# Optimization experiments

Hardware: AMD Instinct MI355X
Metric: run time of the kernel (lower is better)

## Reference

```python
import math
import jax, jax.numpy as jnp
import numpy as np

B, S, D, H = 2, 4096, 1024, 16
HD = D // H            # 64 head dim
FFN = 4096             # encoder_ffn_dim = 4*d_model
WIN = 512              # attention_window
w = WIN // 2           # one-sided window = 256
NEG = -1e9


def setup_inputs() -> dict:
    key = jax.random.key(0)
    ks = jax.random.split(key, 16)
    p = lambda k, shape: (jax.random.normal(k, shape, jnp.float32) * 0.02)
    inp = {
        "hidden_states": jax.random.normal(ks[0], (B, S, D), jnp.float32),
        "attention_mask": jnp.zeros((B, S), jnp.float32),
        "layer_head_mask": jnp.ones((H,), jnp.float32),
        "is_index_masked": jnp.zeros((B, S), bool),
        "is_index_global_attn": jnp.zeros((B, S), bool),
        "is_global_attn": 0,
        "Wq": p(ks[1], (D, D)), "bq": jnp.zeros((D,), jnp.float32),
        "Wk": p(ks[2], (D, D)), "bk": jnp.zeros((D,), jnp.float32),
        "Wv": p(ks[3], (D, D)), "bv": jnp.zeros((D,), jnp.float32),
        "Wo": p(ks[4], (D, D)), "bo": jnp.zeros((D,), jnp.float32),
        "ln1_g": jnp.ones((D,), jnp.float32), "ln1_b": jnp.zeros((D,), jnp.float32),
        "W1": p(ks[5], (D, FFN)), "b1": jnp.zeros((FFN,), jnp.float32),
        "W2": p(ks[6], (FFN, D)), "b2": jnp.zeros((D,), jnp.float32),
        "ln2_g": jnp.ones((D,), jnp.float32), "ln2_b": jnp.zeros((D,), jnp.float32),
    }
    return inp


def _ln(x, g, b, eps=1e-5):
    m = x.mean(-1, keepdims=True)
    v = ((x - m) ** 2).mean(-1, keepdims=True)
    return (x - m) * jax.lax.rsqrt(v + eps) * g + b


def _blocks3(x, nb, pad_val=0.0):
    # x: [B, H, S, d] -> [B, H, nb, 3w, d]: key blocks b-1, b, b+1 per query block b
    xp = jnp.pad(x, ((0, 0), (0, 0), (w, w), (0, 0)), constant_values=pad_val)
    xb = xp.reshape(x.shape[0], x.shape[1], nb + 2, w, x.shape[-1])
    return jnp.concatenate([xb[:, :, i:i + nb] for i in range(3)], axis=3)


def _sliding_window_attn(q, k, v, key_mask_add, is_masked_q, head_mask):
    # q,k,v: [B, H, S, hd]; banded attention |i-j| <= w
    b, h, s, hd = q.shape
    nb = s // w
    qb = (q * (1.0 / math.sqrt(hd))).reshape(b, h, nb, w, hd)
    kb = _blocks3(k, nb)
    vb = _blocks3(v, nb)
    scores = jnp.einsum("bhnqd,bhnkd->bhnqk", qb, kb)  # [B,H,nb,w,3w]
    # additive key mask (padding keys get NEG)
    kmp = jnp.pad(key_mask_add, ((0, 0), (w, w)), constant_values=NEG)
    kmp = kmp.reshape(b, nb + 2, w)
    km = jnp.concatenate([kmp[:, i:i + nb] for i in range(3)], axis=2)  # [B,nb,3w]
    scores = scores + km[:, None, :, None, :]
    qi = jnp.arange(w)[:, None]
    ki = jnp.arange(3 * w)[None, :]
    band = jnp.abs(ki - w - qi) <= w  # [w, 3w]
    scores = jnp.where(band, scores, NEG)
    probs = jax.nn.softmax(scores, axis=-1)
    probs = probs * head_mask[None, :, None, None, None]
    probs = jnp.where(is_masked_q.reshape(b, 1, nb, w, 1), 0.0, probs)
    out = jnp.einsum("bhnqk,bhnkd->bhnqd", probs, vb)
    return out.reshape(b, h, s, hd)


def reference(hidden_states, attention_mask, layer_head_mask, is_index_masked,
              is_index_global_attn, is_global_attn,
              Wq, bq, Wk, bk, Wv, bv, Wo, bo, ln1_g, ln1_b,
              W1, b1, W2, b2, ln2_g, ln2_b):
    hs = hidden_states
    split = lambda x: (x).reshape(B, S, H, HD).transpose(0, 2, 1, 3)  # [B,H,S,hd]
    q = split(hs @ Wq + bq)
    k = split(hs @ Wk + bk)
    v = split(hs @ Wv + bv)
    attn = _sliding_window_attn(q, k, v, attention_mask, is_index_masked, layer_head_mask)
    attn = attn.transpose(0, 2, 1, 3).reshape(B, S, D)
    attn = attn @ Wo + bo  # self_attn output projection
    x = _ln(hs + attn, ln1_g, ln1_b)
    h = jax.nn.gelu(x @ W1 + b1, approximate=False)
    h = h @ W2 + b2
    x = _ln(x + h, ln2_g, ln2_b)
    return x
```

## Files before the change

kernel.cpp:

```cpp
#include <hip/hip_runtime.h>


typedef unsigned short ushort_t;
typedef unsigned char uchar_t;
typedef __attribute__((ext_vector_type(8))) short bf16x8;
typedef __attribute__((ext_vector_type(4))) float f32x4;

constexpr int CB  = 2;
constexpr int CS  = 4096;
constexpr int CD  = 1024;
constexpr int CH  = 16;
constexpr int CHD = 64;
constexpr int CF  = 4096;
constexpr int CM  = CB * CS;
constexpr float NEGV = -1e9f;

__device__ __forceinline__ ushort_t f2bf(float f) {
  unsigned u = __float_as_uint(f);
  unsigned r = u + 0x7FFFu + ((u >> 16) & 1u);
  return (ushort_t)(r >> 16);
}
__device__ __forceinline__ float gelu_exact(float x) {
  return 0.5f * x * (1.0f + erff(x * 0.70710678118654752f));
}

__device__ __forceinline__ bf16x8 ldsfrag(const char* lds, int row, int slot) {
  return *(const bf16x8*)(lds + row * 128 + (((slot ^ (row & 7)) << 4)));
}

template <int NROWS>
__device__ __forceinline__ void stage_swz(const ushort_t* __restrict__ src, int stride,
                                          char* lds, int tid) {
  const int lane = tid & 63, w = tid >> 6;
#pragma unroll
  for (int it = 0; it < NROWS / 32; ++it) {
    const int o   = it * 4096 + w * 1024;
    const int eo  = o + lane * 16;
    const int row = eo >> 7;
    const int lslot = ((eo >> 4) & 7) ^ (row & 7);
    const ushort_t* g = src + (size_t)row * stride + lslot * 8;
    __builtin_amdgcn_global_load_lds((const __attribute__((address_space(1))) void*)g,
                                     (__attribute__((address_space(3))) void*)(lds + o),
                                     16, 0, 0);
  }
}

__device__ __forceinline__ void stageC(const ushort_t* __restrict__ gtile, int ldK,
                                       char* ldsT, int chunk, int tid) {
  const int eo   = chunk * 8192 + tid * 16;
  const int row  = eo >> 7;
  const int slot = ((eo >> 4) & 7) ^ (row & 7);
  __builtin_amdgcn_global_load_lds(
      (const __attribute__((address_space(1))) void*)(gtile + (size_t)row * ldK + slot * 8),
      (__attribute__((address_space(3))) void*)(ldsT + eo), 16, 0, 0);
}

template <int MH, int NH, int NPH, int NF, int VM, typename F>
__device__ __forceinline__ void phase8(const char* Ax, const char* Bx,
                                       int wr, int wc, int rl, int kl,
                                       f32x4 (&acc)[8][NF], F stage) {
  bf16x8 af[4][2], bfr[NPH][2];
#pragma unroll
  for (int mf = 0; mf < 4; ++mf)
#pragma unroll
    for (int kk = 0; kk < 2; ++kk)
      af[mf][kk] = ldsfrag(Ax, wr * 128 + (MH * 4 + mf) * 16 + rl, kk * 4 + kl);
#pragma unroll
  for (int nf = 0; nf < NPH; ++nf)
#pragma unroll
    for (int kk = 0; kk < 2; ++kk)
      bfr[nf][kk] = ldsfrag(Bx, wc * (NF * 16) + (NH * NPH + nf) * 16 + rl, kk * 4 + kl);
  stage();
  __builtin_amdgcn_s_barrier();
  asm volatile("s_waitcnt lgkmcnt(0)" ::: "memory");
  __builtin_amdgcn_s_setprio(1);
#pragma unroll
  for (int mf = 0; mf < 4; ++mf)
#pragma unroll
    for (int nf = 0; nf < NPH; ++nf)
#pragma unroll
      for (int kk = 0; kk < 2; ++kk)
        acc[MH * 4 + mf][NH * NPH + nf] = __builtin_amdgcn_mfma_f32_16x16x32_bf16(
            af[mf][kk], bfr[nf][kk], acc[MH * 4 + mf][NH * NPH + nf], 0, 0, 0);
  __builtin_amdgcn_s_setprio(0);
  if constexpr (VM == 1) asm volatile("s_waitcnt vmcnt(2)" ::: "memory");
  if constexpr (VM == 2) asm volatile("s_waitcnt vmcnt(0)" ::: "memory");
  __builtin_amdgcn_s_barrier();
}

template <int BN>
__device__ __forceinline__ void run_mainloop(const ushort_t* __restrict__ A,
                                             const ushort_t* __restrict__ Bt,
                                             int K, int bm, int bn, char* lds, int tid,
                                             f32x4 (&acc)[8][BN / 64]) {
  constexpr int NF = BN / 64;
  char* Ab0 = lds;
  char* Bb0 = lds + 32768;
  char* Ab1 = lds + 32768 + BN * 128;
  char* Bb1 = Ab1 + 32768;
  const int lane = tid & 63, wid = tid >> 6;
  const int wr = wid >> 2, wc = wid & 3, rl = lane & 15, kl = lane >> 4;
  const ushort_t* Ao = A + (size_t)bm * K;
  const ushort_t* Bo = Bt + (size_t)bn * K;
  const int NT = K >> 6;
#pragma unroll
  for (int c = 0; c < 4; ++c) stageC(Ao, K, Ab0, c, tid);
#pragma unroll
  for (int c = 0; c < NF; ++c) stageC(Bo, K, Bb0, c, tid);
  if (NT > 1) {
    stageC(Ao + 64, K, Ab1, 0, tid);
    stageC(Ao + 64, K, Ab1, 2, tid);
    asm volatile("s_waitcnt vmcnt(2)" ::: "memory");
  } else {
    asm volatile("s_waitcnt vmcnt(0)" ::: "memory");
  }
  __builtin_amdgcn_s_barrier();

  for (int m = 0; m < NT; ++m) {
    const int p = m & 1;
    char* Ax = p ? Ab1 : Ab0;  char* Bx = p ? Bb1 : Bb0;
    char* Axn = p ? Ab0 : Ab1; char* Bxn = p ? Bb0 : Bb1;
    const bool s1 = (m + 1 < NT), s2 = (m + 2 < NT);
    const ushort_t* An1 = Ao + (m + 1) * 64;
    const ushort_t* Bn1 = Bo + (m + 1) * 64;
    const ushort_t* An2 = Ao + (m + 2) * 64;
    if constexpr (NF == 4) {
      phase8<0, 0, 2, 4, 0>(Ax, Bx, wr, wc, rl, kl, acc, [&] {
        if (s1) { stageC(An1, K, Axn, 1, tid); stageC(An1, K, Axn, 3, tid); } });
      phase8<0, 1, 2, 4, 0>(Ax, Bx, wr, wc, rl, kl, acc, [&] {
        if (s1) { stageC(Bn1, K, Bxn, 0, tid); stageC(Bn1, K, Bxn, 1, tid); } });
      phase8<1, 0, 2, 4, 0>(Ax, Bx, wr, wc, rl, kl, acc, [&] {
        if (s1) { stageC(Bn1, K, Bxn, 2, tid); stageC(Bn1, K, Bxn, 3, tid); } });
      if (s2)      phase8<1, 1, 2, 4, 1>(Ax, Bx, wr, wc, rl, kl, acc, [&] {
        stageC(An2, K, Ax, 0, tid); stageC(An2, K, Ax, 2, tid); });
      else if (s1) phase8<1, 1, 2, 4, 2>(Ax, Bx, wr, wc, rl, kl, acc, [&] {});
      else         phase8<1, 1, 2, 4, 0>(Ax, Bx, wr, wc, rl, kl, acc, [&] {});
    } else {
      phase8<0, 0, 2, 2, 0>(Ax, Bx, wr, wc, rl, kl, acc, [&] {
        if (s1) { stageC(An1, K, Axn, 1, tid); stageC(An1, K, Axn, 3, tid);
                  stageC(Bn1, K, Bxn, 0, tid); } });
      if (s2)      phase8<1, 0, 2, 2, 1>(Ax, Bx, wr, wc, rl, kl, acc, [&] {
        stageC(Bn1, K, Bxn, 1, tid);
        stageC(An2, K, Ax, 0, tid); stageC(An2, K, Ax, 2, tid); });
      else if (s1) phase8<1, 0, 2, 2, 2>(Ax, Bx, wr, wc, rl, kl, acc, [&] {
        stageC(Bn1, K, Bxn, 1, tid); });
      else         phase8<1, 0, 2, 2, 0>(Ax, Bx, wr, wc, rl, kl, acc, [&] {});
    }
  }
}

template <int BN, int EPI>
__global__ __launch_bounds__(512, 1) void gemm8(
    const ushort_t* __restrict__ A, const ushort_t* __restrict__ Bt,
    const float* __restrict__ bias, const float* __restrict__ res,
    float* __restrict__ outF, ushort_t* __restrict__ outB, int N, int K) {
  constexpr int NF = BN / 64;
  __shared__ __align__(16) char lds[2 * (32768 + BN * 128)];
  const int tid = threadIdx.x;
  const int bm = blockIdx.x * 256, bn = blockIdx.y * BN;
  f32x4 acc[8][NF] = {};
  run_mainloop<BN>(A, Bt, K, bm, bn, lds, tid, acc);
  const int lane = tid & 63, wid = tid >> 6;
  const int wr = wid >> 2, wc = wid & 3, rl = lane & 15, kl = lane >> 4;
#pragma unroll
  for (int mf = 0; mf < 8; ++mf) {
    const int r0 = bm + wr * 128 + mf * 16 + kl * 4;
#pragma unroll
    for (int nf = 0; nf < NF; ++nf) {
      const int col = bn + wc * (NF * 16) + nf * 16 + rl;
      const float bb = bias[col];
#pragma unroll
      for (int i = 0; i < 4; ++i) {
        float v = acc[mf][nf][i] + bb;
        if (EPI == 1) {
          v += res[(size_t)(r0 + i) * N + col];
          outF[(size_t)(r0 + i) * N + col] = v;
        } else {
          outB[(size_t)(r0 + i) * N + col] = f2bf(gelu_exact(v));
        }
      }
    }
  }
}

__global__ __launch_bounds__(512, 1) void qkv8(
    const ushort_t* __restrict__ hsb,
    const ushort_t* __restrict__ WqT, const ushort_t* __restrict__ WkT,
    const ushort_t* __restrict__ WvT,
    const float* __restrict__ bq, const float* __restrict__ bk, const float* __restrict__ bv,
    ushort_t* __restrict__ q, ushort_t* __restrict__ k, ushort_t* __restrict__ vt) {
  __shared__ __align__(16) char lds[2 * (32768 + 16384)];
  const int tid = threadIdx.x;
  const int which = blockIdx.z;
  const ushort_t* Wt = (which == 0) ? WqT : (which == 1) ? WkT : WvT;
  const float* bia   = (which == 0) ? bq  : (which == 1) ? bk  : bv;
  const float mul    = (which == 0) ? 0.125f : 1.0f;
  const int bm = blockIdx.x * 256, bn = blockIdx.y * 128;
  f32x4 acc[8][2] = {};
  run_mainloop<128>(hsb, Wt, CD, bm, bn, lds, tid, acc);
  const int lane = tid & 63, wid = tid >> 6;
  const int wr = wid >> 2, wc = wid & 3, rl = lane & 15, kl = lane >> 4;
#pragma unroll
  for (int mf = 0; mf < 8; ++mf) {
    const int r0 = bm + wr * 128 + mf * 16 + kl * 4;
    const int bidx = r0 >> 12;
    const int s0 = r0 & (CS - 1);
#pragma unroll
    for (int nf = 0; nf < 2; ++nf) {
      const int col = bn + wc * 32 + nf * 16 + rl;
      const int h = col >> 6, hd = col & 63;
      const float bb = bia[col];
      if (which < 2) {
        ushort_t* dst = (which == 0 ? q : k);
#pragma unroll
        for (int i = 0; i < 4; ++i) {
          const float v = (acc[mf][nf][i] + bb) * mul;
          dst[((((size_t)bidx * CH + h) * CS) + s0 + i) * CHD + hd] = f2bf(v);
        }
      } else {
        ushort4 o;
        o.x = f2bf(acc[mf][nf][0] + bb); o.y = f2bf(acc[mf][nf][1] + bb);
        o.z = f2bf(acc[mf][nf][2] + bb); o.w = f2bf(acc[mf][nf][3] + bb);
        *(ushort4*)&vt[(((size_t)bidx * CH + h) * CHD + hd) * CS + s0] = o;
      }
    }
  }
}

__global__ __launch_bounds__(256) void cast_bf16(const float* __restrict__ x,
                                                 ushort_t* __restrict__ y) {
  const size_t i = ((size_t)blockIdx.x * 256 + threadIdx.x) * 4;
  const float4 v = *(const float4*)(x + i);
  ushort4 o;
  o.x = f2bf(v.x); o.y = f2bf(v.y); o.z = f2bf(v.z); o.w = f2bf(v.w);
  *(ushort4*)(y + i) = o;
}

__global__ __launch_bounds__(256) void transpose_cast(const float* __restrict__ W,
                                                      ushort_t* __restrict__ Wt,
                                                      int K, int N) {
  __shared__ float t[64][65];
  const int k0 = blockIdx.x * 64, n0 = blockIdx.y * 64;
  const int ty = threadIdx.x >> 4, tx = threadIdx.x & 15;
#pragma unroll
  for (int rr = 0; rr < 4; ++rr) {
    const int r = rr * 16 + ty;
    const float4 v = *(const float4*)&W[(size_t)(k0 + r) * N + n0 + tx * 4];
    t[r][tx * 4 + 0] = v.x; t[r][tx * 4 + 1] = v.y;
    t[r][tx * 4 + 2] = v.z; t[r][tx * 4 + 3] = v.w;
  }
  __syncthreads();
#pragma unroll
  for (int rr = 0; rr < 4; ++rr) {
    const int rn = rr * 16 + ty;
    ushort4 o;
    o.x = f2bf(t[tx * 4 + 0][rn]); o.y = f2bf(t[tx * 4 + 1][rn]);
    o.z = f2bf(t[tx * 4 + 2][rn]); o.w = f2bf(t[tx * 4 + 3][rn]);
    *(ushort4*)&Wt[(size_t)(n0 + rn) * K + k0 + tx * 4] = o;
  }
}

__global__ __launch_bounds__(256) void attn_mfma(
    const ushort_t* __restrict__ qg, const ushort_t* __restrict__ kg,
    const ushort_t* __restrict__ vtg,
    const float* __restrict__ amask, const uchar_t* __restrict__ qmask,
    const float* __restrict__ hmask, ushort_t* __restrict__ outb) {
  __shared__ __align__(16) char Qs[8192];
  __shared__ __align__(16) char Ks[8192];
  __shared__ __align__(16) char Vt[8192];
  __shared__ __align__(16) char Ps[8192];
  const int qt0 = blockIdx.x * 64, h = blockIdx.y, b = blockIdx.z;
  const int tid = threadIdx.x, lane = tid & 63, w = tid >> 6;
  const size_t bh = (size_t)b * CH + h;

  stage_swz<64>(qg + (bh * CS + qt0) * CHD, CHD, Qs, tid);

  f32x4 O[4] = {};
  float m_run[4], l_run[4];
#pragma unroll
  for (int i = 0; i < 4; ++i) { m_run[i] = -INFINITY; l_run[i] = 0.f; }

  for (int c = 0; c < 9; ++c) {
    const int k0 = qt0 - 256 + c * 64;
    if (k0 < 0 || k0 >= CS) continue;
    __syncthreads();
    stage_swz<64>(kg + (bh * CS + k0) * CHD, CHD, Ks, tid);
    stage_swz<64>(vtg + bh * CHD * CS + k0, CS, Vt, tid);
    __syncthreads();

    f32x4 s[4] = {};
#pragma unroll
    for (int kk = 0; kk < 2; ++kk) {
      const bf16x8 a = ldsfrag(Qs, w * 16 + (lane & 15), kk * 4 + (lane >> 4));
#pragma unroll
      for (int n = 0; n < 4; ++n) {
        const bf16x8 bb = ldsfrag(Ks, n * 16 + (lane & 15), kk * 4 + (lane >> 4));
        s[n] = __builtin_amdgcn_mfma_f32_16x16x32_bf16(a, bb, s[n], 0, 0, 0);
      }
    }

    float kmv[4]; int keyc[4];
#pragma unroll
    for (int n = 0; n < 4; ++n) {
      keyc[n] = k0 + n * 16 + (lane & 15);
      kmv[n] = amask[(size_t)b * CS + keyc[n]];
    }
    const int qrb = qt0 + w * 16 + ((lane >> 4) << 2);
#pragma unroll
    for (int i = 0; i < 4; ++i) {
      const int qi = qrb + i;
      float mx = -INFINITY;
#pragma unroll
      for (int n = 0; n < 4; ++n) {
        const int d = keyc[n] - qi;
        float x = (d <= 256 && d >= -256) ? (s[n][i] + kmv[n]) : NEGV;
        s[n][i] = x;
        mx = fmaxf(mx, x);
      }
      mx = fmaxf(mx, __shfl_xor(mx, 1));
      mx = fmaxf(mx, __shfl_xor(mx, 2));
      mx = fmaxf(mx, __shfl_xor(mx, 4));
      mx = fmaxf(mx, __shfl_xor(mx, 8));
      const float m_new = fmaxf(m_run[i], mx);
      const float scf = expf(m_run[i] - m_new);
      float rs = 0.f;
#pragma unroll
      for (int n = 0; n < 4; ++n) {
        const float p = expf(s[n][i] - m_new);
        s[n][i] = p;
        rs += p;
      }
      rs += __shfl_xor(rs, 1); rs += __shfl_xor(rs, 2);
      rs += __shfl_xor(rs, 4); rs += __shfl_xor(rs, 8);
      l_run[i] = l_run[i] * scf + rs;
      m_run[i] = m_new;
#pragma unroll
      for (int n = 0; n < 4; ++n) O[n][i] *= scf;
      const int prow = w * 16 + ((lane >> 4) << 2) + i;
#pragma unroll
      for (int n = 0; n < 4; ++n) {
        const int pcol = n * 16 + (lane & 15);
        const int byte = prow * 128 + ((((pcol >> 3) ^ (prow & 7)) << 4)) + ((pcol & 7) << 1);
        *(ushort_t*)(Ps + byte) = f2bf(s[n][i]);
      }
    }
    __syncthreads();

#pragma unroll
    for (int kk = 0; kk < 2; ++kk) {
      const bf16x8 pa = ldsfrag(Ps, w * 16 + (lane & 15), kk * 4 + (lane >> 4));
#pragma unroll
      for (int nd = 0; nd < 4; ++nd) {
        const bf16x8 vv = ldsfrag(Vt, nd * 16 + (lane & 15), kk * 4 + (lane >> 4));
        O[nd] = __builtin_amdgcn_mfma_f32_16x16x32_bf16(pa, vv, O[nd], 0, 0, 0);
      }
    }
  }

  const float hm = hmask[h];
#pragma unroll
  for (int i = 0; i < 4; ++i) {
    const int qi = qt0 + w * 16 + ((lane >> 4) << 2) + i;
    const bool qm = qmask[(size_t)b * CS + qi] != 0;
    const float scl = (qm ? 0.f : hm) / fmaxf(l_run[i], 1e-30f);
#pragma unroll
    for (int nd = 0; nd < 4; ++nd) {
      const int col = h * CHD + nd * 16 + (lane & 15);
      outb[((size_t)b * CS + qi) * CD + col] = f2bf(O[nd][i] * scl);
    }
  }
}

__global__ __launch_bounds__(256) void ln_f32(const float* __restrict__ X,
                                              const float* __restrict__ g,
                                              const float* __restrict__ bt,
                                              float* __restrict__ Y,
                                              ushort_t* __restrict__ Yb) {
  const int row = blockIdx.x;
  const int tid = threadIdx.x;
  const float4 xv = *(const float4*)(X + (size_t)row * CD + (tid << 2));
  float s  = xv.x + xv.y + xv.z + xv.w;
  float s2 = xv.x * xv.x + xv.y * xv.y + xv.z * xv.z + xv.w * xv.w;
#pragma unroll
  for (int off = 32; off; off >>= 1) {
    s  += __shfl_xor(s, off);
    s2 += __shfl_xor(s2, off);
  }
  __shared__ float red[8];
  const int wv = tid >> 6;
  if ((tid & 63) == 0) { red[wv] = s; red[wv + 4] = s2; }
  __syncthreads();
  s  = red[0] + red[1] + red[2] + red[3];
  s2 = red[4] + red[5] + red[6] + red[7];
  const float mean = s * (1.f / CD);
  const float var  = s2 * (1.f / CD) - mean * mean;
  const float r = rsqrtf(var + 1e-5f);
  const float4 gv = *(const float4*)(g + (tid << 2));
  const float4 bv = *(const float4*)(bt + (tid << 2));
  float4 o;
  o.x = (xv.x - mean) * r * gv.x + bv.x;
  o.y = (xv.y - mean) * r * gv.y + bv.y;
  o.z = (xv.z - mean) * r * gv.z + bv.z;
  o.w = (xv.w - mean) * r * gv.w + bv.w;
  *(float4*)(Y + (size_t)row * CD + (tid << 2)) = o;
  if (Yb) {
    ushort4 ob;
    ob.x = f2bf(o.x); ob.y = f2bf(o.y); ob.z = f2bf(o.z); ob.w = f2bf(o.w);
    *(ushort4*)(Yb + (size_t)row * CD + (tid << 2)) = ob;
  }
}

extern "C" void kernel_launch(void* const* d_in, const int* in_sizes, int n_in,
                              void* d_out, int out_size, void* d_ws, size_t ws_size,
                              hipStream_t stream) {
  const float* hs    = (const float*)d_in[0];
  const float* amask = (const float*)d_in[1];
  const float* hmask = (const float*)d_in[2];
  const uchar_t* qmask = (const uchar_t*)d_in[3];
  const float* Wq = (const float*)d_in[6];
  const float* bq = (const float*)d_in[7];
  const float* Wk = (const float*)d_in[8];
  const float* bk = (const float*)d_in[9];
  const float* Wv = (const float*)d_in[10];
  const float* bv = (const float*)d_in[11];
  const float* Wo = (const float*)d_in[12];
  const float* bo = (const float*)d_in[13];
  const float* ln1g = (const float*)d_in[14];
  const float* ln1b = (const float*)d_in[15];
  const float* W1 = (const float*)d_in[16];
  const float* b1 = (const float*)d_in[17];
  const float* W2 = (const float*)d_in[18];
  const float* b2 = (const float*)d_in[19];
  const float* ln2g = (const float*)d_in[20];
  const float* ln2b = (const float*)d_in[21];

  char* ws = (char*)d_ws;
  const size_t MB = 1024 * 1024;
  ushort_t* hsb  = (ushort_t*)(ws);
  ushort_t* WqT  = (ushort_t*)(ws + 16 * MB);
  ushort_t* WkT  = (ushort_t*)(ws + 18 * MB);
  ushort_t* WvT  = (ushort_t*)(ws + 20 * MB);
  ushort_t* WoT  = (ushort_t*)(ws + 22 * MB);
  ushort_t* W1T  = (ushort_t*)(ws + 24 * MB);
  ushort_t* W2T  = (ushort_t*)(ws + 32 * MB);
  ushort_t* qb   = (ushort_t*)(ws + 40 * MB);
  ushort_t* kb   = (ushort_t*)(ws + 56 * MB);
  ushort_t* vtb  = (ushort_t*)(ws + 72 * MB);
  ushort_t* attb = (ushort_t*)(ws + 88 * MB);
  float*    tmp  = (float*)(ws + 104 * MB);
  float*    x1   = (float*)(ws + 40 * MB);
  ushort_t* x1b  = (ushort_t*)(ws + 72 * MB);
  ushort_t* hb   = (ushort_t*)(ws + 136 * MB);
  float*    outf = (float*)d_out;

  cast_bf16<<<(CM * CD) / 1024, 256, 0, stream>>>(hs, hsb);
  transpose_cast<<<dim3(CD / 64, CD / 64), 256, 0, stream>>>(Wq, WqT, CD, CD);
  transpose_cast<<<dim3(CD / 64, CD / 64), 256, 0, stream>>>(Wk, WkT, CD, CD);
  transpose_cast<<<dim3(CD / 64, CD / 64), 256, 0, stream>>>(Wv, WvT, CD, CD);
  transpose_cast<<<dim3(CD / 64, CD / 64), 256, 0, stream>>>(Wo, WoT, CD, CD);
  transpose_cast<<<dim3(CD / 64, CF / 64), 256, 0, stream>>>(W1, W1T, CD, CF);
  transpose_cast<<<dim3(CF / 64, CD / 64), 256, 0, stream>>>(W2, W2T, CF, CD);

  qkv8<<<dim3(CM / 256, CD / 128, 3), 512, 0, stream>>>(
      hsb, WqT, WkT, WvT, bq, bk, bv, qb, kb, vtb);

  attn_mfma<<<dim3(CS / 64, CH, CB), 256, 0, stream>>>(
      qb, kb, vtb, amask, qmask, hmask, attb);

  gemm8<128, 1><<<dim3(CM / 256, CD / 128), 512, 0, stream>>>(
      attb, WoT, bo, hs, tmp, nullptr, CD, CD);

  ln_f32<<<CM, 256, 0, stream>>>(tmp, ln1g, ln1b, x1, x1b);

  gemm8<256, 2><<<dim3(CM / 256, CF / 256), 512, 0, stream>>>(
      x1b, W1T, b1, nullptr, nullptr, hb, CF, CD);

  gemm8<128, 1><<<dim3(CM / 256, CD / 128), 512, 0, stream>>>(
      hb, W2T, b2, x1, outf, nullptr, CD, CF);

  ln_f32<<<CM, 256, 0, stream>>>(outf, ln2g, ln2b, outf, nullptr);
}
```

Measured before the change: 569.2 us.

## Reschedule GEMM prefetch order, add workgroup swizzle, merge QKV weights into one GEMM

Reorders the global-to-LDS staging in the GEMM mainloop so B tiles are loaded before A, and retunes the vmcnt wait thresholds per phase. For BN=256 the prefetch depth drops to a single stage with a full wait in the prologue. Adds a workgroup-ID swizzle that interleaves tiles across groups of 8, aiming at better L2 reuse across XCDs. The three QKV weights are packed into one contiguous transposed matrix so qkv8 runs as a single 2D grid. The changed waits trade deeper prefetch for simpler ordering, which risks stalls if the new vmcnt counts are off.

```diff
diff --git a/kernel.cpp b/kernel.cpp
--- a/kernel.cpp
+++ b/kernel.cpp
@@ -83,8 +83,10 @@
         acc[MH * 4 + mf][NH * NPH + nf] = __builtin_amdgcn_mfma_f32_16x16x32_bf16(
             af[mf][kk], bfr[nf][kk], acc[MH * 4 + mf][NH * NPH + nf], 0, 0, 0);
   __builtin_amdgcn_s_setprio(0);
-  if constexpr (VM == 1) asm volatile("s_waitcnt vmcnt(2)" ::: "memory");
-  if constexpr (VM == 2) asm volatile("s_waitcnt vmcnt(0)" ::: "memory");
+  if constexpr (VM == 0) asm volatile("s_waitcnt vmcnt(0)" ::: "memory");
+  if constexpr (VM == 2) asm volatile("s_waitcnt vmcnt(2)" ::: "memory");
+  if constexpr (VM == 4) asm volatile("s_waitcnt vmcnt(4)" ::: "memory");
+  if constexpr (VM == 6) asm volatile("s_waitcnt vmcnt(6)" ::: "memory");
   __builtin_amdgcn_s_barrier();
 }
 
@@ -103,16 +105,24 @@
   const ushort_t* Ao = A + (size_t)bm * K;
   const ushort_t* Bo = Bt + (size_t)bn * K;
   const int NT = K >> 6;
-#pragma unroll
-  for (int c = 0; c < 4; ++c) stageC(Ao, K, Ab0, c, tid);
-#pragma unroll
-  for (int c = 0; c < NF; ++c) stageC(Bo, K, Bb0, c, tid);
-  if (NT > 1) {
-    stageC(Ao + 64, K, Ab1, 0, tid);
-    stageC(Ao + 64, K, Ab1, 2, tid);
-    asm volatile("s_waitcnt vmcnt(2)" ::: "memory");
+
+  if constexpr (NF == 4) {
+#pragma unroll
+    for (int c = 0; c < 4; ++c) stageC(Bo, K, Bb0, c, tid);
+#pragma unroll
+    for (int c = 0; c < 4; ++c) stageC(Ao, K, Ab0, c, tid);
+    asm volatile("s_waitcnt vmcnt(0)" ::: "memory");
   } else {
-    asm volatile("s_waitcnt vmcnt(0)" ::: "memory");
+    stageC(Bo, K, Bb0, 0, tid); stageC(Bo, K, Bb0, 1, tid);
+#pragma unroll
+    for (int c = 0; c < 4; ++c) stageC(Ao, K, Ab0, c, tid);
+    if (NT > 1) {
+      stageC(Ao + 64, K, Ab1, 0, tid);
+      stageC(Ao + 64, K, Ab1, 2, tid);
+      asm volatile("s_waitcnt vmcnt(2)" ::: "memory");
+    } else {
+      asm volatile("s_waitcnt vmcnt(0)" ::: "memory");
+    }
   }
   __builtin_amdgcn_s_barrier();
 
@@ -125,28 +135,36 @@
     const ushort_t* Bn1 = Bo + (m + 1) * 64;
     const ushort_t* An2 = Ao + (m + 2) * 64;
     if constexpr (NF == 4) {
-      phase8<0, 0, 2, 4, 0>(Ax, Bx, wr, wc, rl, kl, acc, [&] {
+      phase8<0, 0, 2, 4, -1>(Ax, Bx, wr, wc, rl, kl, acc, [&] {
+        if (s1) { stageC(Bn1, K, Bxn, 0, tid); stageC(Bn1, K, Bxn, 1, tid);
+                  stageC(Bn1, K, Bxn, 2, tid); stageC(Bn1, K, Bxn, 3, tid); } });
+      if (s1) phase8<0, 1, 2, 4, 6>(Ax, Bx, wr, wc, rl, kl, acc, [&] {
+        stageC(An1, K, Axn, 0, tid); stageC(An1, K, Axn, 2, tid); });
+      else    phase8<0, 1, 2, 4, 0>(Ax, Bx, wr, wc, rl, kl, acc, [&] {});
+      phase8<1, 0, 2, 4, -1>(Ax, Bx, wr, wc, rl, kl, acc, [&] {
         if (s1) { stageC(An1, K, Axn, 1, tid); stageC(An1, K, Axn, 3, tid); } });
-      phase8<0, 1, 2, 4, 0>(Ax, Bx, wr, wc, rl, kl, acc, [&] {
-        if (s1) { stageC(Bn1, K, Bxn, 0, tid); stageC(Bn1, K, Bxn, 1, tid); } });
-      phase8<1, 0, 2, 4, 0>(Ax, Bx, wr, wc, rl, kl, acc, [&] {
-        if (s1) { stageC(Bn1, K, Bxn, 2, tid); stageC(Bn1, K, Bxn, 3, tid); } });
-      if (s2)      phase8<1, 1, 2, 4, 1>(Ax, Bx, wr, wc, rl, kl, acc, [&] {
+      if (s1) phase8<1, 1, 2, 4, 2>(Ax, Bx, wr, wc, rl, kl, acc, [&] {});
+      else    phase8<1, 1, 2, 4, 0>(Ax, Bx, wr, wc, rl, kl, acc, [&] {});
+    } else {
+      if (s1) phase8<0, 0, 2, 2, 6>(Ax, Bx, wr, wc, rl, kl, acc, [&] {
+        stageC(Bn1, K, Bxn, 0, tid); stageC(Bn1, K, Bxn, 1, tid);
+        stageC(An1, K, Axn, 1, tid); stageC(An1, K, Axn, 3, tid); });
+      else    phase8<0, 0, 2, 2, 0>(Ax, Bx, wr, wc, rl, kl, acc, [&] {});
+      if (s2)      phase8<1, 0, 2, 2, 4>(Ax, Bx, wr, wc, rl, kl, acc, [&] {
         stageC(An2, K, Ax, 0, tid); stageC(An2, K, Ax, 2, tid); });
-      else if (s1) phase8<1, 1, 2, 4, 2>(Ax, Bx, wr, wc, rl, kl, acc, [&] {});
-      else         phase8<1, 1, 2, 4, 0>(Ax, Bx, wr, wc, rl, kl, acc, [&] {});
-    } else {
-      phase8<0, 0, 2, 2, 0>(Ax, Bx, wr, wc, rl, kl, acc, [&] {
-        if (s1) { stageC(An1, K, Axn, 1, tid); stageC(An1, K, Axn, 3, tid);
-                  stageC(Bn1, K, Bxn, 0, tid); } });
-      if (s2)      phase8<1, 0, 2, 2, 1>(Ax, Bx, wr, wc, rl, kl, acc, [&] {
-        stageC(Bn1, K, Bxn, 1, tid);
-        stageC(An2, K, Ax, 0, tid); stageC(An2, K, Ax, 2, tid); });
-      else if (s1) phase8<1, 0, 2, 2, 2>(Ax, Bx, wr, wc, rl, kl, acc, [&] {
-        stageC(Bn1, K, Bxn, 1, tid); });
+      else if (s1) phase8<1, 0, 2, 2, 2>(Ax, Bx, wr, wc, rl, kl, acc, [&] {});
       else         phase8<1, 0, 2, 2, 0>(Ax, Bx, wr, wc, rl, kl, acc, [&] {});
     }
   }
+}
+
+__device__ __forceinline__ void swz_block(int BN, int& bm, int& bn) {
+  const int gx = gridDim.x;
+  const int nwg = gx * gridDim.y;
+  const int id0 = blockIdx.x + gx * blockIdx.y;
+  const int wgid = (id0 & 7) * (nwg >> 3) + (id0 >> 3);
+  bm = (wgid % gx) * 256;
+  bn = (wgid / gx) * BN;
 }
 
 template <int BN, int EPI>
@@ -157,7 +175,7 @@
   constexpr int NF = BN / 64;
   __shared__ __align__(16) char lds[2 * (32768 + BN * 128)];
   const int tid = threadIdx.x;
-  const int bm = blockIdx.x * 256, bn = blockIdx.y * BN;
+  int bm, bn; swz_block(BN, bm, bn);
   f32x4 acc[8][NF] = {};
   run_mainloop<BN>(A, Bt, K, bm, bn, lds, tid, acc);
   const int lane = tid & 63, wid = tid >> 6;
@@ -184,20 +202,18 @@
 }
 
 __global__ __launch_bounds__(512, 1) void qkv8(
-    const ushort_t* __restrict__ hsb,
-    const ushort_t* __restrict__ WqT, const ushort_t* __restrict__ WkT,
-    const ushort_t* __restrict__ WvT,
+    const ushort_t* __restrict__ hsb, const ushort_t* __restrict__ WqkvT,
     const float* __restrict__ bq, const float* __restrict__ bk, const float* __restrict__ bv,
     ushort_t* __restrict__ q, ushort_t* __restrict__ k, ushort_t* __restrict__ vt) {
   __shared__ __align__(16) char lds[2 * (32768 + 16384)];
   const int tid = threadIdx.x;
-  const int which = blockIdx.z;
-  const ushort_t* Wt = (which == 0) ? WqT : (which == 1) ? WkT : WvT;
-  const float* bia   = (which == 0) ? bq  : (which == 1) ? bk  : bv;
-  const float mul    = (which == 0) ? 0.125f : 1.0f;
-  const int bm = blockIdx.x * 256, bn = blockIdx.y * 128;
+  int bm, bn; swz_block(128, bm, bn);
+  const int which = bn >> 10;
+  const int bnl = bn & 1023;
+  const float* bia = (which == 0) ? bq : (which == 1) ? bk : bv;
+  const float mul  = (which == 0) ? 0.125f : 1.0f;
   f32x4 acc[8][2] = {};
-  run_mainloop<128>(hsb, Wt, CD, bm, bn, lds, tid, acc);
+  run_mainloop<128>(hsb, WqkvT, CD, bm, bn, lds, tid, acc);
   const int lane = tid & 63, wid = tid >> 6;
   const int wr = wid >> 2, wc = wid & 3, rl = lane & 15, kl = lane >> 4;
 #pragma unroll
@@ -207,7 +223,7 @@
     const int s0 = r0 & (CS - 1);
 #pragma unroll
     for (int nf = 0; nf < 2; ++nf) {
-      const int col = bn + wc * 32 + nf * 16 + rl;
+      const int col = bnl + wc * 32 + nf * 16 + rl;
       const int h = col >> 6, hd = col & 63;
       const float bb = bia[col];
       if (which < 2) {
@@ -436,33 +452,31 @@
 
   char* ws = (char*)d_ws;
   const size_t MB = 1024 * 1024;
-  ushort_t* hsb  = (ushort_t*)(ws);
-  ushort_t* WqT  = (ushort_t*)(ws + 16 * MB);
-  ushort_t* WkT  = (ushort_t*)(ws + 18 * MB);
-  ushort_t* WvT  = (ushort_t*)(ws + 20 * MB);
-  ushort_t* WoT  = (ushort_t*)(ws + 22 * MB);
-  ushort_t* W1T  = (ushort_t*)(ws + 24 * MB);
-  ushort_t* W2T  = (ushort_t*)(ws + 32 * MB);
-  ushort_t* qb   = (ushort_t*)(ws + 40 * MB);
-  ushort_t* kb   = (ushort_t*)(ws + 56 * MB);
-  ushort_t* vtb  = (ushort_t*)(ws + 72 * MB);
-  ushort_t* attb = (ushort_t*)(ws + 88 * MB);
-  float*    tmp  = (float*)(ws + 104 * MB);
-  float*    x1   = (float*)(ws + 40 * MB);
-  ushort_t* x1b  = (ushort_t*)(ws + 72 * MB);
-  ushort_t* hb   = (ushort_t*)(ws + 136 * MB);
-  float*    outf = (float*)d_out;
+  ushort_t* hsb   = (ushort_t*)(ws);
+  ushort_t* WqkvT = (ushort_t*)(ws + 16 * MB);
+  ushort_t* WoT   = (ushort_t*)(ws + 22 * MB);
+  ushort_t* W1T   = (ushort_t*)(ws + 24 * MB);
+  ushort_t* W2T   = (ushort_t*)(ws + 32 * MB);
+  ushort_t* qb    = (ushort_t*)(ws + 40 * MB);
+  ushort_t* kb    = (ushort_t*)(ws + 56 * MB);
+  ushort_t* vtb   = (ushort_t*)(ws + 72 * MB);
+  ushort_t* attb  = (ushort_t*)(ws + 88 * MB);
+  float*    tmp   = (float*)(ws + 104 * MB);
+  float*    x1    = (float*)(ws + 40 * MB);
+  ushort_t* x1b   = (ushort_t*)(ws + 72 * MB);
+  ushort_t* hb    = (ushort_t*)(ws + 136 * MB);
+  float*    outf  = (float*)d_out;
 
   cast_bf16<<<(CM * CD) / 1024, 256, 0, stream>>>(hs, hsb);
-  transpose_cast<<<dim3(CD / 64, CD / 64), 256, 0, stream>>>(Wq, WqT, CD, CD);
-  transpose_cast<<<dim3(CD / 64, CD / 64), 256, 0, stream>>>(Wk, WkT, CD, CD);
-  transpose_cast<<<dim3(CD / 64, CD / 64), 256, 0, stream>>>(Wv, WvT, CD, CD);
+  transpose_cast<<<dim3(CD / 64, CD / 64), 256, 0, stream>>>(Wq, WqkvT, CD, CD);
+  transpose_cast<<<dim3(CD / 64, CD / 64), 256, 0, stream>>>(Wk, WqkvT + 1024 * 1024, CD, CD);
+  transpose_cast<<<dim3(CD / 64, CD / 64), 256, 0, stream>>>(Wv, WqkvT + 2 * 1024 * 1024, CD, CD);
   transpose_cast<<<dim3(CD / 64, CD / 64), 256, 0, stream>>>(Wo, WoT, CD, CD);
   transpose_cast<<<dim3(CD / 64, CF / 64), 256, 0, stream>>>(W1, W1T, CD, CF);
   transpose_cast<<<dim3(CF / 64, CD / 64), 256, 0, stream>>>(W2, W2T, CF, CD);
 
-  qkv8<<<dim3(CM / 256, CD / 128, 3), 512, 0, stream>>>(
-      hsb, WqT, WkT, WvT, bq, bk, bv, qb, kb, vtb);
+  qkv8<<<dim3(CM / 256, 3072 / 128), 512, 0, stream>>>(
+      hsb, WqkvT, bq, bk, bv, qb, kb, vtb);
 
   attn_mfma<<<dim3(CS / 64, CH, CB), 256, 0, stream>>>(
       qb, kb, vtb, amask, qmask, hmask, attb);
```

After: 601.8 us. 1.06x slower.
